# Kernel tuning notes

Hardware: AMD Instinct MI355X
Metric: run time of the kernel (lower is better)

The kernel has to match this reference:

```python
import jax, jax.numpy as jnp
import numpy as np

TEMPERATURE = 10.0
EPS = 1e-12  # torch F.normalize eps


def setup_inputs() -> dict:
    key = jax.random.key(0)
    k1, k2 = jax.random.split(key)
    B, D = 8192, 1024
    text_embeddings = jax.random.normal(k1, (B, D), dtype=jnp.float32)
    image_embeddings = jax.random.normal(k2, (B, D), dtype=jnp.float32)
    bias = jnp.zeros((1,), dtype=jnp.float32)
    return {
        "text_embeddings": text_embeddings,
        "image_embeddings": image_embeddings,
        "bias": bias,
    }


def _normalize(x):
    # matches torch F.normalize(p=2, dim=1): x / max(||x||, eps)
    norm = jnp.linalg.norm(x, axis=-1, keepdims=True)
    return x / jnp.maximum(norm, EPS)


def reference(text_embeddings, image_embeddings, bias):
    B = text_embeddings.shape[0]
    img_n = _normalize(image_embeddings)   # [B, D]
    txt_n = _normalize(text_embeddings)    # [B, D]
    # similarity[i, j] = <img_i, txt_j>
    sim = jnp.einsum('id,jd->ij', img_n, txt_n)          # [B, B]
    logits = sim * (-TEMPERATURE) + bias[0]
    labels = 2.0 * jnp.eye(B, dtype=logits.dtype) - 1.0   # +1 diag, -1 off-diag
    # loss_ij = log(1/(1+exp(label*logit))) = -softplus(label*logit)
    total_loss = -jnp.sum(jax.nn.softplus(labels * logits))
    return -(total_loss / B)
```

## Files before the change

kernel.cpp:

```cpp
#include <hip/hip_runtime.h>
#include <stdint.h>
#include <stddef.h>

#define NROWS 8192
#define DIM   1024
#define RB    512
#define TEMP  10.0f

#define BM 256
#define BN 256
#define BK 128
#define NT (DIM / BK)

typedef __attribute__((ext_vector_type(8))) int i32x8;
typedef __attribute__((ext_vector_type(16))) float floatx16;

#define FENCE() asm volatile("" ::: "memory")
#define BARRIER() do { FENCE(); __builtin_amdgcn_s_barrier(); FENCE(); } while (0)

__device__ __forceinline__ void load16_lds(const unsigned char* g, unsigned char* l) {
    __builtin_amdgcn_global_load_lds(
        (__attribute__((address_space(1))) void*)(g),
        (__attribute__((address_space(3))) void*)(l),
        16, 0, 0);
}

__device__ __forceinline__ unsigned fp4q(float x) {
    float a = fabsf(x);
    a = fminf(a, 6.0f);
    unsigned c = (unsigned)(a >= 0.25f) + (unsigned)(a >= 0.75f)
               + (unsigned)(a >= 1.25f) + (unsigned)(a >= 1.75f)
               + (unsigned)(a >= 2.5f)  + (unsigned)(a >= 3.5f)
               + (unsigned)(a >= 5.0f);
    return c | ((__float_as_uint(x) >> 28) & 8u);
}

__device__ __forceinline__ i32x8 op8(int4 lo) {
    union { i32x8 v; int4 q[2]; } u;
    u.q[0] = lo;
    u.q[1] = make_int4(0, 0, 0, 0);
    return u.v;
}


__global__ __launch_bounds__(256) void normalize_kernel(
    const float* __restrict__ img, const float* __restrict__ txt,
    unsigned char* __restrict__ imgq, unsigned char* __restrict__ txtq,
    float* __restrict__ out)
{
    __shared__ __align__(16) unsigned short sc[4][256];
    const int t = threadIdx.x;
    const int lane = t & 63, wave = t >> 6;
    const int gw = blockIdx.x * 4 + wave;
    const float* src = (gw < NROWS) ? img + (size_t)gw * DIM
                                    : txt + (size_t)(gw - NROWS) * DIM;
    float4 v[4];
    float ss = 0.f;
#pragma unroll
    for (int c = 0; c < 4; c++) {
        v[c] = ((const float4*)src)[lane + 64 * c];
        ss += v[c].x * v[c].x + v[c].y * v[c].y + v[c].z * v[c].z + v[c].w * v[c].w;
    }
#pragma unroll
    for (int off = 32; off; off >>= 1) ss += __shfl_xor(ss, off);
    const float scale = 32.0f / fmaxf(sqrtf(ss), 1e-12f);
#pragma unroll
    for (int c = 0; c < 4; c++) {
        unsigned p = fp4q(v[c].x * scale)
                   | (fp4q(v[c].y * scale) << 4)
                   | (fp4q(v[c].z * scale) << 8)
                   | (fp4q(v[c].w * scale) << 12);
        sc[wave][c * 64 + lane] = (unsigned short)p;
    }
    __syncthreads();
    if (t < 128) {
        const int rr = t & 3, k = t >> 2;
        const int gr0 = blockIdx.x * 4;
        unsigned char* dq = (gr0 < NROWS) ? imgq : txtq;
        const int r = (gr0 < NROWS ? gr0 : gr0 - NROWS) + rr;
        const int4 d = *(const int4*)&sc[rr][k * 8];
        const int it = k >> 2, ks = (k >> 1) & 1, fh = k & 1;
        *(int4*)(dq + (size_t)it * 524288 + (size_t)((r >> 5) * 2048
                 + ks * 1024 + fh * 512 + (r & 31) * 16)) = d;
    }
    if (gw == 0 && lane == 0) out[0] = 0.f;
}

__global__ __launch_bounds__(512, 2) void simloss_kernel(
    const unsigned char* __restrict__ An,
    const unsigned char* __restrict__ Bn,
    const float* __restrict__ bias,
    float* __restrict__ out)
{
    __shared__ __align__(16) unsigned char smem[3 * 32768];
    __shared__ float red[24];

    const int t = threadIdx.x;
    const int lane = t & 63;
    const int wave = t >> 6;

    const int bid = blockIdx.x;
    const int blockN = (bid & 7) + 8 * ((bid >> 3) & 3);
    const int blockM = bid >> 5;

    const unsigned char* gA = An + blockM * 16384 + t * 16;
    const unsigned char* gB = Bn + blockN * 16384 + t * 16;

    const int waveM = (wave >> 2) * 128;
    const int waveN = (wave & 3) * 64;
    const int rgA = (wave >> 2) * 4;
    const int cgB = (wave & 3) * 2;
    const int fr = lane & 31;
    const int fh = lane >> 5;

    floatx16 acc[4][2];
#pragma unroll
    for (int mi = 0; mi < 4; mi++)
#pragma unroll
        for (int ni = 0; ni < 2; ni++)
            acc[mi][ni] = (floatx16)(0.f);

    load16_lds(gA, smem + t * 16);
    load16_lds(gA + 8192, smem + t * 16 + 8192);
    load16_lds(gB, smem + 16384 + t * 16);
    load16_lds(gB + 8192, smem + 16384 + t * 16 + 8192);
    load16_lds(gA + 524288, smem + 32768 + t * 16);
    load16_lds(gA + 524288 + 8192, smem + 32768 + t * 16 + 8192);
    load16_lds(gB + 524288, smem + 32768 + 16384 + t * 16);
    load16_lds(gB + 524288 + 8192, smem + 32768 + 16384 + t * 16 + 8192);
    asm volatile("s_waitcnt vmcnt(4)" ::: "memory");
    BARRIER();

#pragma unroll
    for (int it = 0; it < NT; ++it) {
        const int buf = it % 3;
        const int pbuf = (it + 2) % 3;
        const unsigned char* Lw = smem + buf * 32768 + lane * 16;
#pragma unroll
        for (int ks = 0; ks < 2; ++ks) {
            int4 aF[4], bF[2];
#pragma unroll
            for (int mi = 0; mi < 4; mi++)
                aF[mi] = *(const int4*)(Lw + (rgA + mi) * 2048 + ks * 1024);
#pragma unroll
            for (int ni = 0; ni < 2; ni++)
                bF[ni] = *(const int4*)(Lw + 16384 + (cgB + ni) * 2048 + ks * 1024);

            if (it < NT - 2) {
                const size_t ko = (size_t)(it + 2) * 524288;
                unsigned char* Ld = smem + pbuf * 32768 + t * 16;
                if (ks == 0) {
                    load16_lds(gA + ko, Ld);
                    load16_lds(gA + ko + 8192, Ld + 8192);
                } else {
                    load16_lds(gB + ko, Ld + 16384);
                    load16_lds(gB + ko + 8192, Ld + 24576);
                }
            }
            if (ks == 1) {
                if (it < NT - 2) {
                    asm volatile("s_waitcnt vmcnt(4)" ::: "memory");
                } else if (it == NT - 2) {
                    asm volatile("s_waitcnt vmcnt(0)" ::: "memory");
                }
            }
            BARRIER();

            i32x8 a8[4], b8[2];
#pragma unroll
            for (int mi = 0; mi < 4; mi++) a8[mi] = op8(aF[mi]);
#pragma unroll
            for (int ni = 0; ni < 2; ni++) b8[ni] = op8(bF[ni]);

            asm volatile("s_setprio 1");
#pragma unroll
            for (int mi = 0; mi < 4; mi++)
#pragma unroll
                for (int ni = 0; ni < 2; ni++)
                    acc[mi][ni] = __builtin_amdgcn_mfma_scale_f32_32x32x64_f8f6f4(
                        a8[mi], b8[ni], acc[mi][ni],
                        4, 4,
                        0, 0x7f7f7f7f,
                        0, 0x7f7f7f7f);
            asm volatile("s_setprio 0");
            BARRIER();
        }
    }

    const float bv = bias[0];
    const float c1 = -TEMP * 1.4426950408889634f / 1024.0f;
    const float c0 = bv * 1.4426950408889634f;
    float accP = 0.f, accQ = 0.f, accD = 0.f;
    const int gi0 = blockM * BM + waveM + 4 * fh;
    const int gj0 = blockN * BN + waveN + fr;
#pragma unroll
    for (int mi = 0; mi < 4; mi++) {
#pragma unroll
        for (int ni = 0; ni < 2; ni++) {
#pragma unroll
            for (int reg = 0; reg < 16; reg++) {
                float s = acc[mi][ni][reg];
                float w = fmaf(s, c1, c0);
                float e2 = __builtin_amdgcn_exp2f(-fabsf(w));
                accP += __builtin_amdgcn_logf(1.0f + e2);
                accP = fmaf(0.5f, fabsf(w), accP);
                accQ += s;
            }
        }
    }
    const bool diagblk = (blockN == blockM);
    if (diagblk) {
#pragma unroll
        for (int mi = 0; mi < 4; mi++)
#pragma unroll
            for (int ni = 0; ni < 2; ni++)
#pragma unroll
                for (int reg = 0; reg < 16; reg++) {
                    int ig = gi0 + mi * 32 + (reg & 3) + 8 * (reg >> 2);
                    int jg = gj0 + ni * 32;
                    if (ig == jg) accD += acc[mi][ni][reg];
                }
    }
#pragma unroll
    for (int off = 32; off; off >>= 1) {
        accP += __shfl_xor(accP, off);
        accQ += __shfl_xor(accQ, off);
        accD += __shfl_xor(accD, off);
    }
    if (lane == 0) {
        red[wave * 3 + 0] = accP;
        red[wave * 3 + 1] = accQ;
        red[wave * 3 + 2] = accD;
    }
    __syncthreads();
    if (t == 0) {
        float P = 0.f, Q = 0.f, D = 0.f;
#pragma unroll
        for (int w = 0; w < 8; w++) {
            P += red[w * 3 + 0];
            Q += red[w * 3 + 1];
            D += red[w * 3 + 2];
        }
        Q *= (1.0f / 1024.0f);
        D *= (1.0f / 1024.0f);
        float contrib = fmaf(0.6931471805599453f, P, fmaf(5.0f, Q, -32768.0f * bv));
        if (diagblk) contrib += fmaf(-TEMP, D, 256.0f * bv);
        atomicAdd(out, contrib * (1.0f / 8192.0f));
    }
}

extern "C" void kernel_launch(void* const* d_in, const int* in_sizes, int n_in,
                              void* d_out, int out_size, void* d_ws, size_t ws_size,
                              hipStream_t stream) {
    const float* txt = (const float*)d_in[0];
    const float* img = (const float*)d_in[1];
    const float* bias = (const float*)d_in[2];
    float* out = (float*)d_out;

    unsigned char* imgq = (unsigned char*)d_ws;
    unsigned char* txtq = imgq + (size_t)NROWS * RB;

    normalize_kernel<<<dim3(2 * NROWS / 4), dim3(256), 0, stream>>>(
        img, txt, imgq, txtq, out);

    simloss_kernel<<<dim3((NROWS / BM) * (NROWS / BN)), dim3(512), 0, stream>>>(
        imgq, txtq, bias, out);
}
```

Measured before the change: 142.6 us.

## Keep A panel resident in LDS and stream B fragments from global into registers

Each block now loads its full 256-row A panel across all of K into LDS once, then loops over four N tiles spaced eight apart. B fragments are read straight from global memory into registers with one-step double buffering, which removes the LDS staging and barriers for B. The grid shrinks to 256 blocks, each with 128 KB of LDS, so A is reused across four output tiles. The cost is that global-load latency is covered only by one MFMA step of prefetch, and occupancy drops to one block per CU.

```diff
diff --git a/kernel.cpp b/kernel.cpp
--- a/kernel.cpp
+++ b/kernel.cpp
@@ -14,9 +14,6 @@
 
 typedef __attribute__((ext_vector_type(8))) int i32x8;
 typedef __attribute__((ext_vector_type(16))) float floatx16;
-
-#define FENCE() asm volatile("" ::: "memory")
-#define BARRIER() do { FENCE(); __builtin_amdgcn_s_barrier(); FENCE(); } while (0)
 
 __device__ __forceinline__ void load16_lds(const unsigned char* g, unsigned char* l) {
     __builtin_amdgcn_global_load_lds(
@@ -33,13 +30,6 @@
                + (unsigned)(a >= 2.5f)  + (unsigned)(a >= 3.5f)
                + (unsigned)(a >= 5.0f);
     return c | ((__float_as_uint(x) >> 28) & 8u);
-}
-
-__device__ __forceinline__ i32x8 op8(int4 lo) {
-    union { i32x8 v; int4 q[2]; } u;
-    u.q[0] = lo;
-    u.q[1] = make_int4(0, 0, 0, 0);
-    return u.v;
 }
 
 
@@ -92,19 +82,29 @@
     const float* __restrict__ bias,
     float* __restrict__ out)
 {
-    __shared__ __align__(16) unsigned char smem[3 * 32768];
-    __shared__ float red[24];
+    __shared__ __align__(16) unsigned char As[8 * 16384];
+    __shared__ float red[4][8];
 
     const int t = threadIdx.x;
     const int lane = t & 63;
     const int wave = t >> 6;
 
     const int bid = blockIdx.x;
-    const int blockN = (bid & 7) + 8 * ((bid >> 3) & 3);
-    const int blockM = bid >> 5;
-
-    const unsigned char* gA = An + blockM * 16384 + t * 16;
-    const unsigned char* gB = Bn + blockN * 16384 + t * 16;
+    const int blockM = bid >> 3;
+    const int n0 = bid & 3 ? (bid & 7) : (bid & 7);
+
+    {
+        const unsigned char* gA = An + (size_t)blockM * 16384 + t * 16;
+#pragma unroll
+        for (int it = 0; it < 8; it++) {
+#pragma unroll
+            for (int j = 0; j < 2; j++)
+                load16_lds(gA + (size_t)it * 524288 + j * 8192,
+                           As + it * 16384 + j * 8192 + t * 16);
+        }
+    }
+    asm volatile("s_waitcnt vmcnt(0)" ::: "memory");
+    __syncthreads();
 
     const int waveM = (wave >> 2) * 128;
     const int waveN = (wave & 3) * 64;
@@ -113,140 +113,126 @@
     const int fr = lane & 31;
     const int fh = lane >> 5;
 
-    floatx16 acc[4][2];
-#pragma unroll
-    for (int mi = 0; mi < 4; mi++)
-#pragma unroll
-        for (int ni = 0; ni < 2; ni++)
-            acc[mi][ni] = (floatx16)(0.f);
-
-    load16_lds(gA, smem + t * 16);
-    load16_lds(gA + 8192, smem + t * 16 + 8192);
-    load16_lds(gB, smem + 16384 + t * 16);
-    load16_lds(gB + 8192, smem + 16384 + t * 16 + 8192);
-    load16_lds(gA + 524288, smem + 32768 + t * 16);
-    load16_lds(gA + 524288 + 8192, smem + 32768 + t * 16 + 8192);
-    load16_lds(gB + 524288, smem + 32768 + 16384 + t * 16);
-    load16_lds(gB + 524288 + 8192, smem + 32768 + 16384 + t * 16 + 8192);
-    asm volatile("s_waitcnt vmcnt(4)" ::: "memory");
-    BARRIER();
-
-#pragma unroll
-    for (int it = 0; it < NT; ++it) {
-        const int buf = it % 3;
-        const int pbuf = (it + 2) % 3;
-        const unsigned char* Lw = smem + buf * 32768 + lane * 16;
-#pragma unroll
-        for (int ks = 0; ks < 2; ++ks) {
-            int4 aF[4], bF[2];
-#pragma unroll
-            for (int mi = 0; mi < 4; mi++)
-                aF[mi] = *(const int4*)(Lw + (rgA + mi) * 2048 + ks * 1024);
+    i32x8 aT[2][4], bT[2][2];
+#pragma unroll
+    for (int p = 0; p < 2; p++) {
+#pragma unroll
+        for (int mi = 0; mi < 4; mi++) aT[p][mi] = (i32x8)0;
+#pragma unroll
+        for (int ni = 0; ni < 2; ni++) bT[p][ni] = (i32x8)0;
+    }
+
+#define LOADA(P, IT, KS)                                                        \
+    {                                                                           \
+        _Pragma("unroll")                                                       \
+        for (int mi_ = 0; mi_ < 4; mi_++)                                       \
+            *(int4*)&aT[P][mi_] = *(const int4*)(As + (IT) * 16384              \
+                + (rgA + mi_) * 2048 + (KS) * 1024 + lane * 16);                \
+    }
+#define LOADB(P, N, IT, KS)                                                     \
+    {                                                                           \
+        _Pragma("unroll")                                                       \
+        for (int ni_ = 0; ni_ < 2; ni_++)                                       \
+            *(int4*)&bT[P][ni_] = *(const int4*)(Bn + (size_t)(IT) * 524288     \
+                + (size_t)(((N) * 8 + cgB + ni_) * 2048 + (KS) * 1024           \
+                           + lane * 16));                                       \
+    }
+
+    LOADA(0, 0, 0);
+    LOADB(0, n0, 0, 0);
+
+    const float bv = bias[0];
+    const float c1 = -TEMP * 1.4426950408889634f / 1024.0f;
+    const float c0 = bv * 1.4426950408889634f;
+
+#pragma unroll
+    for (int k = 0; k < 4; k++) {
+        const int n = n0 + 8 * k;
+        floatx16 acc[4][2];
+#pragma unroll
+        for (int mi = 0; mi < 4; mi++)
 #pragma unroll
             for (int ni = 0; ni < 2; ni++)
-                bF[ni] = *(const int4*)(Lw + 16384 + (cgB + ni) * 2048 + ks * 1024);
-
-            if (it < NT - 2) {
-                const size_t ko = (size_t)(it + 2) * 524288;
-                unsigned char* Ld = smem + pbuf * 32768 + t * 16;
-                if (ks == 0) {
-                    load16_lds(gA + ko, Ld);
-                    load16_lds(gA + ko + 8192, Ld + 8192);
-                } else {
-                    load16_lds(gB + ko, Ld + 16384);
-                    load16_lds(gB + ko + 8192, Ld + 24576);
-                }
+                acc[mi][ni] = (floatx16)(0.f);
+
+#pragma unroll
+        for (int ss = 0; ss < 16; ss++) {
+            const int s = k * 16 + ss;
+            const int p = s & 1;
+            if (s < 63) {
+                const int s1 = s + 1;
+                const int it1 = (s1 >> 1) & 7;
+                const int ks1 = s1 & 1;
+                const int n1 = n0 + 8 * (s1 >> 4);
+                LOADA(p ^ 1, it1, ks1);
+                LOADB(p ^ 1, n1, it1, ks1);
             }
-            if (ks == 1) {
-                if (it < NT - 2) {
-                    asm volatile("s_waitcnt vmcnt(4)" ::: "memory");
-                } else if (it == NT - 2) {
-                    asm volatile("s_waitcnt vmcnt(0)" ::: "memory");
-                }
-            }
-            BARRIER();
-
-            i32x8 a8[4], b8[2];
-#pragma unroll
-            for (int mi = 0; mi < 4; mi++) a8[mi] = op8(aF[mi]);
-#pragma unroll
-            for (int ni = 0; ni < 2; ni++) b8[ni] = op8(bF[ni]);
-
-            asm volatile("s_setprio 1");
 #pragma unroll
             for (int mi = 0; mi < 4; mi++)
 #pragma unroll
                 for (int ni = 0; ni < 2; ni++)
                     acc[mi][ni] = __builtin_amdgcn_mfma_scale_f32_32x32x64_f8f6f4(
-                        a8[mi], b8[ni], acc[mi][ni],
+                        aT[p][mi], bT[p][ni], acc[mi][ni],
                         4, 4,
                         0, 0x7f7f7f7f,
                         0, 0x7f7f7f7f);
-            asm volatile("s_setprio 0");
-            BARRIER();
-        }
-    }
-
-    const float bv = bias[0];
-    const float c1 = -TEMP * 1.4426950408889634f / 1024.0f;
-    const float c0 = bv * 1.4426950408889634f;
-    float accP = 0.f, accQ = 0.f, accD = 0.f;
-    const int gi0 = blockM * BM + waveM + 4 * fh;
-    const int gj0 = blockN * BN + waveN + fr;
-#pragma unroll
-    for (int mi = 0; mi < 4; mi++) {
-#pragma unroll
-        for (int ni = 0; ni < 2; ni++) {
-#pragma unroll
-            for (int reg = 0; reg < 16; reg++) {
-                float s = acc[mi][ni][reg];
-                float w = fmaf(s, c1, c0);
-                float e2 = __builtin_amdgcn_exp2f(-fabsf(w));
-                accP += __builtin_amdgcn_logf(1.0f + e2);
-                accP = fmaf(0.5f, fabsf(w), accP);
-                accQ += s;
+        }
+
+        float accP = 0.f, accQ = 0.f, accD = 0.f;
+        const int gi0 = blockM * BM + waveM + 4 * fh;
+        const int gj0 = n * BN + waveN + fr;
+#pragma unroll
+        for (int mi = 0; mi < 4; mi++) {
+#pragma unroll
+            for (int ni = 0; ni < 2; ni++) {
+#pragma unroll
+                for (int reg = 0; reg < 16; reg++) {
+                    float sv = acc[mi][ni][reg];
+                    float w = fmaf(sv, c1, c0);
+                    float e2 = __builtin_amdgcn_exp2f(-fabsf(w));
+                    accP += __builtin_amdgcn_logf(1.0f + e2);
+                    accP = fmaf(0.5f, fabsf(w), accP);
+                    accQ += sv;
+                }
             }
         }
-    }
-    const bool diagblk = (blockN == blockM);
-    if (diagblk) {
-#pragma unroll
-        for (int mi = 0; mi < 4; mi++)
-#pragma unroll
-            for (int ni = 0; ni < 2; ni++)
-#pragma unroll
-                for (int reg = 0; reg < 16; reg++) {
-                    int ig = gi0 + mi * 32 + (reg & 3) + 8 * (reg >> 2);
-                    int jg = gj0 + ni * 32;
-                    if (ig == jg) accD += acc[mi][ni][reg];
-                }
-    }
-#pragma unroll
-    for (int off = 32; off; off >>= 1) {
-        accP += __shfl_xor(accP, off);
-        accQ += __shfl_xor(accQ, off);
-        accD += __shfl_xor(accD, off);
-    }
-    if (lane == 0) {
-        red[wave * 3 + 0] = accP;
-        red[wave * 3 + 1] = accQ;
-        red[wave * 3 + 2] = accD;
-    }
-    __syncthreads();
-    if (t == 0) {
-        float P = 0.f, Q = 0.f, D = 0.f;
-#pragma unroll
-        for (int w = 0; w < 8; w++) {
-            P += red[w * 3 + 0];
-            Q += red[w * 3 + 1];
-            D += red[w * 3 + 2];
-        }
-        Q *= (1.0f / 1024.0f);
-        D *= (1.0f / 1024.0f);
-        float contrib = fmaf(0.6931471805599453f, P, fmaf(5.0f, Q, -32768.0f * bv));
-        if (diagblk) contrib += fmaf(-TEMP, D, 256.0f * bv);
-        atomicAdd(out, contrib * (1.0f / 8192.0f));
-    }
+        const bool diagblk = (n == blockM);
+        if (diagblk) {
+#pragma unroll
+            for (int mi = 0; mi < 4; mi++)
+#pragma unroll
+                for (int ni = 0; ni < 2; ni++)
+#pragma unroll
+                    for (int reg = 0; reg < 16; reg++) {
+                        int ig = gi0 + mi * 32 + (reg & 3) + 8 * (reg >> 2);
+                        int jg = gj0 + ni * 32;
+                        if (ig == jg) accD += acc[mi][ni][reg];
+                    }
+        }
+#pragma unroll
+        for (int off = 32; off; off >>= 1) {
+            accP += __shfl_xor(accP, off);
+            accQ += __shfl_xor(accQ, off);
+            accD += __shfl_xor(accD, off);
+        }
+        if (lane == 0) {
+            float wcon = fmaf(0.6931471805599453f, accP,
+                              fmaf(5.0f / 1024.0f, accQ,
+                                   diagblk ? (-TEMP / 1024.0f) * accD : 0.f));
+            red[k][wave] = wcon;
+        }
+        __syncthreads();
+        if (t == 0) {
+            float sum = 0.f;
+#pragma unroll
+            for (int w = 0; w < 8; w++) sum += red[k][w];
+            sum += -32768.0f * bv;
+            if (diagblk) sum += 256.0f * bv;
+            atomicAdd(out, sum * (1.0f / 8192.0f));
+        }
+    }
+#undef LOADA
+#undef LOADB
 }
 
 extern "C" void kernel_launch(void* const* d_in, const int* in_sizes, int n_in,
@@ -263,6 +249,6 @@
     normalize_kernel<<<dim3(2 * NROWS / 4), dim3(256), 0, stream>>>(
         img, txt, imgq, txtq, out);
 
-    simloss_kernel<<<dim3((NROWS / BM) * (NROWS / BN)), dim3(512), 0, stream>>>(
+    simloss_kernel<<<dim3(256), dim3(512), 0, stream>>>(
         imgq, txtq, bias, out);
 }
```

Measured after the change: 146.1 us. +2.4%, slower.
